# Optimization experiments

Measured on AMD Instinct MI355X. Metric: run time of the kernel, lower is better.

Reference implementation:

```python
import jax, jax.numpy as jnp
import numpy as np

IN_C, HEAD_C, EXPAND_C, OUT_C, TIME_C, H = 512, 64, 2048, 512, 256, 8
EPS = 1e-5

def _layernorm(x, g, b):
    mu = jnp.mean(x, axis=-1, keepdims=True)
    var = jnp.mean((x - mu) ** 2, axis=-1, keepdims=True)
    return (x - mu) * jax.lax.rsqrt(var + EPS) * g + b

def setup_inputs() -> dict:
    key = jax.random.key(0)
    ks = jax.random.split(key, 12)
    B, N = 4, 2048
    qkv_dim = HEAD_C * H * 2 + IN_C * H
    def lin(k, fan_in, fan_out):
        bound = 1.0 / np.sqrt(fan_in)
        kw, kb = jax.random.split(k)
        W = jax.random.uniform(kw, (fan_in, fan_out), jnp.float32, -bound, bound)
        b = jax.random.uniform(kb, (fan_out,), jnp.float32, -bound, bound)
        return W, b
    qkv_w, qkv_b = lin(ks[0], IN_C, qkv_dim)
    merge_w, merge_b = lin(ks[1], IN_C * H, IN_C)
    time_w, time_b = lin(ks[2], TIME_C, TIME_C)
    ff1_w, ff1_b = lin(ks[3], IN_C + TIME_C, EXPAND_C)
    ff2_w, ff2_b = lin(ks[4], EXPAND_C, OUT_C)
    return {
        'x': jax.random.normal(ks[5], (B, N, IN_C), jnp.float32),
        't': jax.random.normal(ks[6], (B, TIME_C), jnp.float32),
        'ln1_g': jnp.ones((IN_C,), jnp.float32), 'ln1_b': jnp.zeros((IN_C,), jnp.float32),
        'qkv_w': qkv_w, 'qkv_b': qkv_b,
        'merge_w': merge_w, 'merge_b': merge_b,
        'time_w': time_w, 'time_b': time_b,
        'ln2_g': jnp.ones((IN_C + TIME_C,), jnp.float32), 'ln2_b': jnp.zeros((IN_C + TIME_C,), jnp.float32),
        'ff1_w': ff1_w, 'ff1_b': ff1_b,
        'ff2_w': ff2_w, 'ff2_b': ff2_b,
    }

def reference(x, t, ln1_g, ln1_b, qkv_w, qkv_b, merge_w, merge_b,
              time_w, time_b, ln2_g, ln2_b, ff1_w, ff1_b, ff2_w, ff2_b):
    B, N, _ = x.shape
    scale = HEAD_C ** -0.5
    qkv = _layernorm(x, ln1_g, ln1_b) @ qkv_w + qkv_b
    q, k, v = jnp.split(qkv, [HEAD_C * H, 2 * HEAD_C * H], axis=-1)
    q = q.reshape(B, N, H, HEAD_C)          # B N H Cq
    k = k.reshape(B, N, H, HEAD_C)
    v = v.reshape(B, N, H, IN_C)            # V per head has dim in_c (as in source)
    attn = jnp.einsum('bnhc,bmhc->bhnm', q, k) * scale
    attn = jax.nn.softmax(attn, axis=-1)    # dropout = identity (eval)
    out = jnp.einsum('bhnm,bmhd->bnhd', attn, v).reshape(B, N, H * IN_C)
    x = x + out @ merge_w + merge_b
    tt = (t @ time_w + time_b)[:, None, :]  # B 1 time_c, broadcasts over N
    tt = jnp.broadcast_to(tt, (B, N, TIME_C))
    h = _layernorm(jnp.concatenate([x, tt], axis=-1), ln2_g, ln2_b)
    h = jax.nn.gelu(h @ ff1_w + ff1_b, approximate=False)
    return x + (h @ ff2_w + ff2_b)          # shortcut = Identity (in_c == out_c)
```

## Files before the change

### kernel.cpp

```cpp
#include <hip/hip_runtime.h>

#define IN_C 512
#define HEAD_C 64
#define NHEAD 8
#define TIME_C 256
#define EXPAND_C 2048
#define NB 4
#define NN 2048
#define QKV_DIM 5120
#define ROWS (NB*NN)
#define MERGE_K (NHEAD*IN_C)
#define LN2_C (IN_C+TIME_C)

typedef __bf16 bf16x8 __attribute__((ext_vector_type(8)));
typedef float f32x4 __attribute__((ext_vector_type(4)));
typedef float f32x16 __attribute__((ext_vector_type(16)));
typedef unsigned int u32x4 __attribute__((ext_vector_type(4)));

__device__ __forceinline__ unsigned short f2bf(float f){
  unsigned int u = __builtin_bit_cast(unsigned int, f);
  u += 0x7fffu + ((u >> 16) & 1u);
  return (unsigned short)(u >> 16);
}
__device__ __forceinline__ unsigned int cvtpk(float a, float b){
  unsigned int r;
  asm("v_cvt_pk_bf16_f32 %0, %1, %2" : "=v"(r) : "v"(a), "v"(b));
  return r;
}
__device__ __forceinline__ float vexp2(float x){
  float r;
  asm("v_exp_f32 %0, %1" : "=v"(r) : "v"(x));
  return r;
}
__device__ __forceinline__ float bpermf(float v, int srclane){
  int r = __builtin_amdgcn_ds_bpermute(srclane<<2, __builtin_bit_cast(int, v));
  return __builtin_bit_cast(float, r);
}

__global__ __launch_bounds__(256) void k_transpose_w(const float* __restrict__ W,
                                                     unsigned short* __restrict__ Wt,
                                                     int K, int N){
  __shared__ unsigned short tile[64*72];
  int t = threadIdx.x;
  int kb = blockIdx.y<<6, nb = blockIdx.x<<6;
  {
    int kr = t>>2, nc = (t&3)<<4;
    const float* src = W + (size_t)(kb+kr)*N + nb + nc;
    alignas(16) unsigned short tmp[16];
    #pragma unroll
    for (int j=0;j<16;j+=4){
      float4 v = *(const float4*)(src + j);
      tmp[j+0]=f2bf(v.x); tmp[j+1]=f2bf(v.y); tmp[j+2]=f2bf(v.z); tmp[j+3]=f2bf(v.w);
    }
    *(bf16x8*)&tile[kr*72 + nc]     = *(bf16x8*)&tmp[0];
    *(bf16x8*)&tile[kr*72 + nc + 8] = *(bf16x8*)&tmp[8];
  }
  __syncthreads();
  {
    int nr = t>>2, kc = (t&3)<<4;
    alignas(16) unsigned short ov[16];
    #pragma unroll
    for (int i=0;i<16;i++) ov[i] = tile[(kc+i)*72 + nr];
    unsigned short* dst = Wt + (size_t)(nb+nr)*K + kb + kc;
    *(bf16x8*)dst     = *(bf16x8*)&ov[0];
    *(bf16x8*)(dst+8) = *(bf16x8*)&ov[8];
  }
}

__global__ __launch_bounds__(256) void k_repack_k(const unsigned short* __restrict__ qkv,
                                                  unsigned short* __restrict__ Kf){
  __shared__ unsigned short tile[64*72];
  int j = blockIdx.x;
  int kb64 = j&31, bh = j>>5;
  int b = bh>>3, hh = bh&7;
  int t = threadIdx.x;
  {
    int key = t>>2, sc = t&3;
    const unsigned short* src = qkv + (size_t)(b*NN + kb64*64 + key)*QKV_DIM + IN_C + hh*HEAD_C;
    *(bf16x8*)&tile[key*72 + sc*8]     = *(const bf16x8*)(src + sc*8);
    *(bf16x8*)&tile[key*72 + (sc+4)*8] = *(const bf16x8*)(src + (sc+4)*8);
  }
  __syncthreads();
  int l = t&63, w = t>>6;
  int kb32l = w&1, kk0 = w>>1;
  #pragma unroll
  for (int i=0;i<2;i++){
    int kk = kk0 + i*2;
    alignas(16) unsigned short ov[8];
    #pragma unroll
    for (int jj=0;jj<8;jj++)
      ov[jj] = tile[(kb32l*32 + (l&31))*72 + kk*16 + (l>>5)*8 + jj];
    size_t dst = (((size_t)(bh*64 + kb64*2 + kb32l))*4 + kk)*512 + l*8;
    *(bf16x8*)(Kf + dst) = *(bf16x8*)ov;
  }
}

__global__ __launch_bounds__(256) void k_repack_v(const unsigned short* __restrict__ qkv,
                                                  unsigned short* __restrict__ Vf){
  __shared__ unsigned short tile[64*136];
  int j = blockIdx.x;
  int kb64 = j&31, bh = j>>5;
  int b = bh>>3, hh = bh&7;
  int t = threadIdx.x, l = t&63, w = t>>6;
  int key = t>>2, sc = t&3;
  const unsigned short* srow = qkv + (size_t)(b*NN + kb64*64 + key)*QKV_DIM + 2*IN_C + hh*IN_C;
  for (int p=0;p<4;p++){
    #pragma unroll
    for (int i=0;i<4;i++){
      int ch = sc + i*4;
      *(bf16x8*)&tile[key*136 + ch*8] = *(const bf16x8*)(srow + p*128 + ch*8);
    }
    __syncthreads();
    #pragma unroll
    for (int dbl=0;dbl<4;dbl++){
      alignas(16) unsigned short ov[8];
      #pragma unroll
      for (int jj=0;jj<8;jj++)
        ov[jj] = tile[(w*16 + (l>>5)*8 + jj)*136 + dbl*32 + (l&31)];
      size_t dst = (((size_t)(bh*128 + kb64*4 + w))*16 + p*4 + dbl)*512 + l*8;
      *(bf16x8*)(Vf + dst) = *(bf16x8*)ov;
    }
    __syncthreads();
  }
}

__global__ __launch_bounds__(256) void k_ln1(const float* __restrict__ x,
                                             const float* __restrict__ g,
                                             const float* __restrict__ bta,
                                             unsigned short* __restrict__ out){
  int row = (blockIdx.x<<2) + (threadIdx.x>>6);
  int l = threadIdx.x&63;
  const float* px = x + (size_t)row*IN_C + l*8;
  alignas(16) float v[8];
  *(float4*)&v[0] = *(const float4*)px;
  *(float4*)&v[4] = *(const float4*)(px+4);
  float s=0.f, sq=0.f;
  #pragma unroll
  for (int j=0;j<8;j++){ s+=v[j]; sq+=v[j]*v[j]; }
  #pragma unroll
  for (int d=32; d>0; d>>=1){ s += __shfl_xor(s,d); sq += __shfl_xor(sq,d); }
  float mu = s*(1.f/IN_C);
  float var = sq*(1.f/IN_C) - mu*mu;
  float rstd = rsqrtf(var + 1e-5f);
  alignas(16) unsigned short o[8];
  #pragma unroll
  for (int j=0;j<8;j++){
    int c = l*8+j;
    o[j] = f2bf((v[j]-mu)*rstd*g[c] + bta[c]);
  }
  *(bf16x8*)(out + (size_t)row*IN_C + l*8) = *(bf16x8*)o;
}

__global__ __launch_bounds__(256) void k_time(const float* __restrict__ t,
                                              const float* __restrict__ W,
                                              const float* __restrict__ bias,
                                              float* __restrict__ tt){
  int b = blockIdx.x, j = threadIdx.x;
  float acc = bias[j];
  const float* tr = t + b*TIME_C;
  #pragma unroll 4
  for (int c=0;c<TIME_C;c++) acc = fmaf(tr[c], W[c*TIME_C + j], acc);
  tt[b*TIME_C + j] = acc;
}

__global__ __launch_bounds__(256) void k_ln2(const float* __restrict__ x2,
                                             const float* __restrict__ tt,
                                             const float* __restrict__ g,
                                             const float* __restrict__ bta,
                                             unsigned short* __restrict__ out){
  int row = (blockIdx.x<<2) + (threadIdx.x>>6);
  int l = threadIdx.x&63;
  int bi = row>>11;
  float v[12];
  int c0 = l*12;
  #pragma unroll
  for (int j=0;j<12;j++){
    int c = c0+j;
    v[j] = (c < IN_C) ? x2[(size_t)row*IN_C + c] : tt[bi*TIME_C + c - IN_C];
  }
  float s=0.f, sq=0.f;
  #pragma unroll
  for (int j=0;j<12;j++){ s+=v[j]; sq+=v[j]*v[j]; }
  #pragma unroll
  for (int d=32; d>0; d>>=1){ s += __shfl_xor(s,d); sq += __shfl_xor(sq,d); }
  float mu = s*(1.f/LN2_C);
  float var = sq*(1.f/LN2_C) - mu*mu;
  float rstd = rsqrtf(var + 1e-5f);
  #pragma unroll
  for (int j=0;j<12;j++){
    int c = c0+j;
    out[(size_t)row*LN2_C + c] = f2bf((v[j]-mu)*rstd*g[c] + bta[c]);
  }
}

template<int EPI>
__global__ __launch_bounds__(256) void k_gemm(const unsigned short* __restrict__ A, int lda,
                                              const unsigned short* __restrict__ Bt, int ldb,
                                              const float* __restrict__ bias,
                                              const float* __restrict__ res, int ldres,
                                              void* __restrict__ Cp, int ldc, int K){
  __shared__ unsigned short sA[128*40];
  __shared__ unsigned short sB[128*40];
  int t = threadIdx.x;
  int l = t&63, w = t>>6;
  int m0 = blockIdx.y<<7, n0 = blockIdx.x<<7;
  int wr = (w>>1)<<6, wc = (w&1)<<6;
  int lm = l&15, kq = (l>>4)<<3;
  f32x4 acc[4][4] = {};
  int sr = t>>2, sc = (t&3)<<3;
  const unsigned short* pA = A + (size_t)(m0+sr)*lda + sc;
  const unsigned short* pB = Bt + (size_t)(n0+sr)*ldb + sc;
  int soff = sr*40 + sc;
  for (int k0=0; k0<K; k0+=32){
    bf16x8 a0 = *(const bf16x8*)pA;
    bf16x8 a1 = *(const bf16x8*)(pA + (size_t)64*lda);
    bf16x8 b0 = *(const bf16x8*)pB;
    bf16x8 b1 = *(const bf16x8*)(pB + (size_t)64*ldb);
    pA += 32; pB += 32;
    __syncthreads();
    *(bf16x8*)&sA[soff]         = a0;
    *(bf16x8*)&sA[soff + 64*40] = a1;
    *(bf16x8*)&sB[soff]         = b0;
    *(bf16x8*)&sB[soff + 64*40] = b1;
    __syncthreads();
    bf16x8 af[4], bfv[4];
    #pragma unroll
    for (int i=0;i<4;i++){
      af[i]  = *(const bf16x8*)&sA[(wr + i*16 + lm)*40 + kq];
      bfv[i] = *(const bf16x8*)&sB[(wc + i*16 + lm)*40 + kq];
    }
    #pragma unroll
    for (int mi=0;mi<4;mi++)
      #pragma unroll
      for (int ni=0;ni<4;ni++)
        acc[mi][ni] = __builtin_amdgcn_mfma_f32_16x16x32_bf16(af[mi], bfv[ni], acc[mi][ni], 0,0,0);
  }
  int lr4 = (l>>4)<<2;
  #pragma unroll
  for (int mi=0;mi<4;mi++){
    int row0 = m0 + wr + mi*16 + lr4;
    #pragma unroll
    for (int ni=0;ni<4;ni++){
      int col = n0 + wc + ni*16 + lm;
      float bi = bias[col];
      #pragma unroll
      for (int r=0;r<4;r++){
        float v = acc[mi][ni][r] + bi;
        int row = row0 + r;
        if (EPI==1){
          v += res[(size_t)row*ldres + col];
          ((float*)Cp)[(size_t)row*ldc + col] = v;
        } else if (EPI==2){
          v = 0.5f*v*(1.f + erff(v*0.70710678118f));
          ((unsigned short*)Cp)[(size_t)row*ldc + col] = f2bf(v);
        } else {
          ((unsigned short*)Cp)[(size_t)row*ldc + col] = f2bf(v);
        }
      }
    }
  }
}

__global__ __launch_bounds__(256, 2) void k_attn(const unsigned short* __restrict__ qkv,
                                                 const unsigned short* __restrict__ Kf,
                                                 const unsigned short* __restrict__ Vf,
                                                 unsigned short* __restrict__ out){
  int j = blockIdx.x;
  int xcd = j&7;
  int rest = j>>3;
  int bh = xcd + ((rest>>6)<<3);
  int inner = rest&63;
  int qb = inner>>2, dh = inner&3;
  int b = bh>>3, hh = bh&7;
  int t = threadIdx.x, l = t&63, w = t>>6;
  int q0 = qb*128 + w*32;
  int lq = l&31, half = l>>5;

  bf16x8 qf[4];
  #pragma unroll
  for (int kk=0;kk<4;kk++)
    qf[kk] = *(const bf16x8*)(qkv + (size_t)(b*NN + q0 + lq)*QKV_DIM + hh*HEAD_C + kk*16 + half*8);

  f32x16 o[4] = {};
  float l_ = 0.f;

  const unsigned short* Kbase = Kf + (size_t)bh*64*2048 + l*8;
  const unsigned short* Vbase = Vf + ((size_t)bh*128*16 + dh*4)*512 + l*8;

  auto loadchunk = [&](int c, bf16x8 (&kfv)[4], bf16x8 (&vfv)[2][4]){
    const unsigned short* kp = Kbase + (size_t)c*2048;
    #pragma unroll
    for (int kk=0;kk<4;kk++)
      kfv[kk] = *(const bf16x8*)(kp + kk*512);
    const unsigned short* vp = Vbase + (size_t)c*16384;
    #pragma unroll
    for (int kc=0;kc<2;kc++)
      #pragma unroll
      for (int dn=0;dn<4;dn++)
        vfv[kc][dn] = *(const bf16x8*)(vp + kc*8192 + dn*512);
  };

  auto body = [&](bf16x8 (&kfv)[4], bf16x8 (&vfv)[2][4]){
    f32x16 s = {};
    s = __builtin_amdgcn_mfma_f32_32x32x16_bf16(kfv[0], qf[0], s, 0,0,0);
    s = __builtin_amdgcn_mfma_f32_32x32x16_bf16(kfv[1], qf[1], s, 0,0,0);
    s = __builtin_amdgcn_mfma_f32_32x32x16_bf16(kfv[2], qf[2], s, 0,0,0);
    s = __builtin_amdgcn_mfma_f32_32x32x16_bf16(kfv[3], qf[3], s, 0,0,0);

    float pv[16]; float ps = 0.f;
    #pragma unroll
    for (int r=0;r<16;r++){
      pv[r] = vexp2(s[r]*0.18033688f);
      ps += pv[r];
    }
    ps += __shfl_xor(ps, 32);
    l_ += ps;

    unsigned int wv[8], xw[8];
    #pragma unroll
    for (int jj=0;jj<8;jj++) wv[jj] = cvtpk(pv[2*jj], pv[2*jj+1]);
    #pragma unroll
    for (int jj=0;jj<8;jj++) xw[jj] = __shfl_xor(wv[jj], 32);
    u32x4 f0 = half ? (u32x4){xw[2],xw[3],wv[2],wv[3]} : (u32x4){wv[0],wv[1],xw[0],xw[1]};
    u32x4 f1 = half ? (u32x4){xw[6],xw[7],wv[6],wv[7]} : (u32x4){wv[4],wv[5],xw[4],xw[5]};
    bf16x8 pf0 = __builtin_bit_cast(bf16x8, f0);
    bf16x8 pf1 = __builtin_bit_cast(bf16x8, f1);

    #pragma unroll
    for (int dn=0;dn<4;dn++){
      o[dn] = __builtin_amdgcn_mfma_f32_32x32x16_bf16(pf0, vfv[0][dn], o[dn], 0,0,0);
      o[dn] = __builtin_amdgcn_mfma_f32_32x32x16_bf16(pf1, vfv[1][dn], o[dn], 0,0,0);
    }
  };

  bf16x8 kfa[4], vfa[2][4], kfb[4], vfb[2][4];
  loadchunk(0, kfa, vfa);
  for (int c=0; c<64; c+=2){
    loadchunk(c+1, kfb, vfb);
    body(kfa, vfa);
    if (c+2 < 64) loadchunk(c+2, kfa, vfa);
    body(kfb, vfb);
  }

  float invl = 1.f / l_;
  #pragma unroll
  for (int r=0;r<16;r++){
    int qr = (r&3) + 8*(r>>2) + 4*half;
    float il = bpermf(invl, qr);
    size_t row = (size_t)(b*NN + q0 + qr);
    #pragma unroll
    for (int dn=0;dn<4;dn++){
      int col = hh*IN_C + dh*128 + dn*32 + lq;
      out[row*MERGE_K + col] = f2bf(o[dn][r]*il);
    }
  }
}

extern "C" void kernel_launch(void* const* d_in, const int* in_sizes, int n_in,
                              void* d_out, int out_size, void* d_ws, size_t ws_size,
                              hipStream_t stream){
  const float* x       = (const float*)d_in[0];
  const float* tin     = (const float*)d_in[1];
  const float* ln1_g   = (const float*)d_in[2];
  const float* ln1_b   = (const float*)d_in[3];
  const float* qkv_w   = (const float*)d_in[4];
  const float* qkv_b   = (const float*)d_in[5];
  const float* merge_w = (const float*)d_in[6];
  const float* merge_b = (const float*)d_in[7];
  const float* time_w  = (const float*)d_in[8];
  const float* time_b  = (const float*)d_in[9];
  const float* ln2_g   = (const float*)d_in[10];
  const float* ln2_b   = (const float*)d_in[11];
  const float* ff1_w   = (const float*)d_in[12];
  const float* ff1_b   = (const float*)d_in[13];
  const float* ff2_w   = (const float*)d_in[14];
  const float* ff2_b   = (const float*)d_in[15];

  char* ws = (char*)d_ws;
  size_t off = 0;
  auto alloc = [&](size_t bytes)->void*{ void* p = ws + off; off += (bytes + 255) & ~(size_t)255; return p; };
  unsigned short* wqkvT   = (unsigned short*)alloc((size_t)QKV_DIM*IN_C*2);
  unsigned short* wmergeT = (unsigned short*)alloc((size_t)IN_C*MERGE_K*2);
  unsigned short* wff1T   = (unsigned short*)alloc((size_t)EXPAND_C*LN2_C*2);
  unsigned short* wff2T   = (unsigned short*)alloc((size_t)IN_C*EXPAND_C*2);
  float*          ttb     = (float*)alloc((size_t)NB*TIME_C*4);
  unsigned short* ln1o    = (unsigned short*)alloc((size_t)ROWS*IN_C*2);
  unsigned short* qkvb    = (unsigned short*)alloc((size_t)ROWS*QKV_DIM*2);
  unsigned short* kfrag   = (unsigned short*)alloc((size_t)32*64*4*64*8*2);
  unsigned short* vfrag   = (unsigned short*)alloc((size_t)32*128*16*64*8*2);
  unsigned short* atto    = (unsigned short*)alloc((size_t)ROWS*MERGE_K*2);
  float*          x2      = (float*)alloc((size_t)ROWS*IN_C*4);
  unsigned short* ln2o = vfrag;
  unsigned short* hbuf = qkvb;

  k_transpose_w<<<dim3(QKV_DIM/64, IN_C/64),  256, 0, stream>>>(qkv_w,   wqkvT,   IN_C,     QKV_DIM);
  k_transpose_w<<<dim3(IN_C/64,   MERGE_K/64),256, 0, stream>>>(merge_w, wmergeT, MERGE_K,  IN_C);
  k_transpose_w<<<dim3(EXPAND_C/64, LN2_C/64),256, 0, stream>>>(ff1_w,   wff1T,   LN2_C,    EXPAND_C);
  k_transpose_w<<<dim3(IN_C/64,   EXPAND_C/64),256, 0, stream>>>(ff2_w,  wff2T,   EXPAND_C, IN_C);
  k_time<<<dim3(NB), 256, 0, stream>>>(tin, time_w, time_b, ttb);
  k_ln1<<<dim3(ROWS/4), 256, 0, stream>>>(x, ln1_g, ln1_b, ln1o);

  k_gemm<0><<<dim3(QKV_DIM/128, ROWS/128), 256, 0, stream>>>(ln1o, IN_C, wqkvT, IN_C, qkv_b, nullptr, 0, qkvb, QKV_DIM, IN_C);
  k_repack_k<<<dim3(1024), 256, 0, stream>>>(qkvb, kfrag);
  k_repack_v<<<dim3(1024), 256, 0, stream>>>(qkvb, vfrag);
  k_attn<<<dim3(2048), 256, 0, stream>>>(qkvb, kfrag, vfrag, atto);
  k_gemm<1><<<dim3(IN_C/128, ROWS/128), 256, 0, stream>>>(atto, MERGE_K, wmergeT, MERGE_K, merge_b, x, IN_C, x2, IN_C, MERGE_K);
  k_ln2<<<dim3(ROWS/4), 256, 0, stream>>>(x2, ttb, ln2_g, ln2_b, ln2o);
  k_gemm<2><<<dim3(EXPAND_C/128, ROWS/128), 256, 0, stream>>>(ln2o, LN2_C, wff1T, LN2_C, ff1_b, nullptr, 0, hbuf, EXPAND_C, LN2_C);
  k_gemm<1><<<dim3(IN_C/128, ROWS/128), 256, 0, stream>>>(hbuf, EXPAND_C, wff2T, EXPAND_C, ff2_b, x2, IN_C, (float*)d_out, IN_C, EXPAND_C);

  (void)in_sizes; (void)n_in; (void)out_size; (void)ws_size;
}
```

Measured before the change: 635.4 us.

## Load GEMM tiles directly into LDS with global_load_lds and use K-step 64

Replaces the register-staged global-to-LDS copy in the generic GEMM with direct global_load_lds transfers of 16 bytes per lane, and doubles the K tile from 32 to 64. Each iteration now issues two MFMA k-steps per barrier pair. The aim is to cut VGPR traffic and ds_write instructions and to halve the number of barriers. The unpadded 64-wide LDS rows (stride 128 bytes) may cause bank conflicts on the fragment reads. The loop also loses the previous overlap of the next global load with the barrier.

```diff
diff --git a/kernel.cpp b/kernel.cpp
--- a/kernel.cpp
+++ b/kernel.cpp
@@ -35,6 +35,11 @@
 __device__ __forceinline__ float bpermf(float v, int srclane){
   int r = __builtin_amdgcn_ds_bpermute(srclane<<2, __builtin_bit_cast(int, v));
   return __builtin_bit_cast(float, r);
+}
+__device__ __forceinline__ void gload16(const unsigned short* g, unsigned short* l){
+  __builtin_amdgcn_global_load_lds(
+      (const __attribute__((address_space(1))) void*)g,
+      (__attribute__((address_space(3))) void*)l, 16, 0, 0);
 }
 
 __global__ __launch_bounds__(256) void k_transpose_w(const float* __restrict__ W,
@@ -199,41 +204,41 @@
                                               const float* __restrict__ bias,
                                               const float* __restrict__ res, int ldres,
                                               void* __restrict__ Cp, int ldc, int K){
-  __shared__ unsigned short sA[128*40];
-  __shared__ unsigned short sB[128*40];
+  __shared__ unsigned short sA[128*64];
+  __shared__ unsigned short sB[128*64];
   int t = threadIdx.x;
   int l = t&63, w = t>>6;
   int m0 = blockIdx.y<<7, n0 = blockIdx.x<<7;
   int wr = (w>>1)<<6, wc = (w&1)<<6;
   int lm = l&15, kq = (l>>4)<<3;
   f32x4 acc[4][4] = {};
-  int sr = t>>2, sc = (t&3)<<3;
-  const unsigned short* pA = A + (size_t)(m0+sr)*lda + sc;
-  const unsigned short* pB = Bt + (size_t)(n0+sr)*ldb + sc;
-  int soff = sr*40 + sc;
-  for (int k0=0; k0<K; k0+=32){
-    bf16x8 a0 = *(const bf16x8*)pA;
-    bf16x8 a1 = *(const bf16x8*)(pA + (size_t)64*lda);
-    bf16x8 b0 = *(const bf16x8*)pB;
-    bf16x8 b1 = *(const bf16x8*)(pB + (size_t)64*ldb);
-    pA += 32; pB += 32;
+  int srow = l>>3, scol = (l&7)<<3;
+  const unsigned short* pA = A + (size_t)m0*lda;
+  const unsigned short* pB = Bt + (size_t)n0*ldb;
+  for (int k0=0; k0<K; k0+=64){
+    #pragma unroll
+    for (int i=0;i<4;i++){
+      int c = w*4 + i;
+      gload16(pA + (size_t)(c*8 + srow)*lda + k0 + scol, &sA[c*512]);
+      gload16(pB + (size_t)(c*8 + srow)*ldb + k0 + scol, &sB[c*512]);
+    }
     __syncthreads();
-    *(bf16x8*)&sA[soff]         = a0;
-    *(bf16x8*)&sA[soff + 64*40] = a1;
-    *(bf16x8*)&sB[soff]         = b0;
-    *(bf16x8*)&sB[soff + 64*40] = b1;
+    bf16x8 af[2][4], bfv[2][4];
+    #pragma unroll
+    for (int kk=0;kk<2;kk++)
+      #pragma unroll
+      for (int i=0;i<4;i++){
+        af[kk][i]  = *(const bf16x8*)&sA[(wr + i*16 + lm)*64 + kk*32 + kq];
+        bfv[kk][i] = *(const bf16x8*)&sB[(wc + i*16 + lm)*64 + kk*32 + kq];
+      }
+    #pragma unroll
+    for (int kk=0;kk<2;kk++)
+      #pragma unroll
+      for (int mi=0;mi<4;mi++)
+        #pragma unroll
+        for (int ni=0;ni<4;ni++)
+          acc[mi][ni] = __builtin_amdgcn_mfma_f32_16x16x32_bf16(af[kk][mi], bfv[kk][ni], acc[mi][ni], 0,0,0);
     __syncthreads();
-    bf16x8 af[4], bfv[4];
-    #pragma unroll
-    for (int i=0;i<4;i++){
-      af[i]  = *(const bf16x8*)&sA[(wr + i*16 + lm)*40 + kq];
-      bfv[i] = *(const bf16x8*)&sB[(wc + i*16 + lm)*40 + kq];
-    }
-    #pragma unroll
-    for (int mi=0;mi<4;mi++)
-      #pragma unroll
-      for (int ni=0;ni<4;ni++)
-        acc[mi][ni] = __builtin_amdgcn_mfma_f32_16x16x32_bf16(af[mi], bfv[ni], acc[mi][ni], 0,0,0);
   }
   int lr4 = (l>>4)<<2;
   #pragma unroll
```

New measurement: 645.4 us. Within noise of the previous version (+1.6%).
